# Kernel optimization log

Measured on AMD Instinct MI355X. Metric: run time of the kernel, lower is better.

Reference implementation:

```python
import jax, jax.numpy as jnp
import numpy as np

DIM, HEADS, DEPTH, SEQ, LOCAL_W = 1024, 16, 7, 2048, 64
HEAD_DIM = DIM // HEADS
SCALE = 1.0 / HEAD_DIM ** 0.5


def cantor_mask(S, depth, local_window):
    """Allowed (i,j): |i-j| within local window, OR |i-j| lies in the Cantor set
    under `depth` levels of ternary subdivision (no base-3 digit equals 1)."""
    idx = np.arange(S)
    d = np.abs(idx[:, None] - idx[None, :])
    x = d.copy()
    ok = np.ones_like(d, dtype=bool)
    for _ in range(depth):
        ok &= (x % 3) != 1
        x //= 3
    ok &= x == 0  # offset must be < 3**depth
    return jnp.asarray(ok | (d <= local_window))  # [S, S] bool


def setup_inputs() -> dict:
    key = jax.random.key(0)
    ks = jax.random.split(key, 8)
    B = 2
    s = 0.02
    return {
        "query": jax.random.normal(ks[0], (B, SEQ, DIM), jnp.float32),
        "key_value": jax.random.normal(ks[1], (B, SEQ, DIM), jnp.float32),
        "Wq": jax.random.normal(ks[2], (DIM, DIM), jnp.float32) * s,
        "bq": jnp.zeros((DIM,), jnp.float32),
        "Wkv": jax.random.normal(ks[3], (DIM, 2 * DIM), jnp.float32) * s,
        "bkv": jnp.zeros((2 * DIM,), jnp.float32),
        "Wo": jax.random.normal(ks[4], (DIM, DIM), jnp.float32) * s,
        "bo": jnp.zeros((DIM,), jnp.float32),
    }


def reference(query, key_value, Wq, bq, Wkv, bkv, Wo, bo):
    B, S, D = query.shape
    H, hd = HEADS, HEAD_DIM
    mask = cantor_mask(S, DEPTH, LOCAL_W)  # static [S, S] bool

    q = (query @ Wq + bq).reshape(B, S, H, hd).transpose(0, 2, 1, 3)  # [B,H,S,hd]
    kv = (key_value @ Wkv + bkv).reshape(B, S, 2, H, hd).transpose(2, 0, 3, 1, 4)
    k, v = kv[0], kv[1]  # [B,H,S,hd]

    scores = jnp.einsum("bhqd,bhkd->bhqk", q, k) * SCALE
    scores = jnp.where(mask, scores, jnp.finfo(scores.dtype).min)
    attn = jax.nn.softmax(scores, axis=-1)
    out = jnp.einsum("bhqk,bhkd->bhqd", attn, v)  # [B,H,S,hd]
    out = out.transpose(0, 2, 1, 3).reshape(B, S, D)
    return out @ Wo + bo
```

## Files before the change

kernel.cpp:

```cpp
#include <hip/hip_runtime.h>
#include <stdint.h>

typedef _Float16 half_t;
typedef __attribute__((ext_vector_type(8))) _Float16 half8;
typedef __attribute__((ext_vector_type(4))) _Float16 half4;
typedef __attribute__((ext_vector_type(4))) float floatx4;

#define SEQ 2048
#define NH 16
#define HD 64

#define MFMA16(a, b, c) __builtin_amdgcn_mfma_f32_16x16x16f16(a, b, c, 0, 0, 0)
#define MFMA32K(a, b, c) __builtin_amdgcn_mfma_f32_16x16x32_f16(a, b, c, 0, 0, 0)

#define QSCALE 0.1803368801111306f

__global__ __launch_bounds__(256) void prep(
    const float* __restrict__ query, const float* __restrict__ key_value,
    const float* __restrict__ Wq, const float* __restrict__ Wkv,
    const float* __restrict__ Wo, half_t* __restrict__ xq,
    half_t* __restrict__ xkv, half_t* __restrict__ wqT,
    half_t* __restrict__ wkvT, half_t* __restrict__ woT,
    uint8_t* __restrict__ tok, uint8_t* __restrict__ tok16,
    uint64_t* __restrict__ maskw) {
  int bx = blockIdx.x, tid = threadIdx.x;
  if (bx < 8192) {
    const float* s; half_t* d; int i;
    if (bx < 4096) { s = query; d = xq; i = (bx * 256 + tid) * 4; }
    else { s = key_value; d = xkv; i = ((bx - 4096) * 256 + tid) * 4; }
    floatx4 v = *(const floatx4*)(s + i);
    half4 h;
    h[0] = (half_t)v[0]; h[1] = (half_t)v[1];
    h[2] = (half_t)v[2]; h[3] = (half_t)v[3];
    *(half4*)(d + i) = h;
    return;
  }
  if (bx < 12288) {
    __shared__ float tile[32][33];
    int id = bx - 8192;
    const float* W; half_t* Wt; int N, nt, kt;
    if (id < 1024) { W = Wq; Wt = wqT; N = 1024; nt = id & 31; kt = id >> 5; }
    else if (id < 3072) { int i2 = id - 1024; W = Wkv; Wt = wkvT; N = 2048; nt = i2 & 63; kt = i2 >> 6; }
    else { int i2 = id - 3072; W = Wo; Wt = woT; N = 1024; nt = i2 & 31; kt = i2 >> 5; }
    const int K = 1024;
    int n0 = nt * 32, k0 = kt * 32;
    int tx = tid & 31, ty = tid >> 5;
#pragma unroll
    for (int i = 0; i < 4; ++i)
      tile[ty + i * 8][tx] = W[(size_t)(k0 + ty + i * 8) * N + n0 + tx];
    __syncthreads();
#pragma unroll
    for (int i = 0; i < 4; ++i)
      Wt[(size_t)(n0 + ty + i * 8) * K + k0 + tx] = (half_t)tile[tx][ty + i * 8];
    return;
  }
  __shared__ uint8_t slut[2048];
  int ib = bx - 12288;
  for (int d = tid; d < 2048; d += 256) {
    int x = d;
    bool ok = true;
    for (int it = 0; it < 7; ++it) { ok &= ((x % 3) != 1); x /= 3; }
    ok &= (x == 0);
    slut[d] = (ok || d <= 64) ? 1 : 0;
  }
  __syncthreads();
  if (ib == 0) {
    if (tid < 64) {
      int delta = tid - 32;
      int lo = delta * 64 - 63, hi = delta * 64 + 63;
      uint8_t any = 0;
      for (int x = lo; x <= hi; ++x) {
        int a = x < 0 ? -x : x;
        if (a < 2048) any |= slut[a];
      }
      tok[tid] = any;
    }
    {
      int d16 = tid - 128;
      int ctr = d16 * 16;
      uint8_t any = 0;
      for (int x = ctr - 15; x <= ctr + 15; ++x) {
        int a = x < 0 ? -x : x;
        if (a < 2048) any |= slut[a];
      }
      tok16[tid] = any;
    }
  }
  int g = ib * 256 + tid;
  int tt = g - 2048;
  uint64_t w = 0;
  for (int jj = 0; jj < 64; ++jj) {
    int d = tt - jj; d = d < 0 ? -d : d;
    if (d < 2048 && slut[d]) w |= (1ull << jj);
  }
  maskw[g] = w;
}

__device__ __forceinline__ void cp16(half_t* lds, const half_t* g) {
  __builtin_amdgcn_global_load_lds(
      (const __attribute__((address_space(1))) uint32_t*)g,
      (__attribute__((address_space(3))) uint32_t*)lds, 16, 0, 0);
}

__global__ __launch_bounds__(256) void gemm_qkv(
    const half_t* __restrict__ xq, const half_t* __restrict__ xkv,
    const half_t* __restrict__ wqT, const half_t* __restrict__ wkvT,
    const float* __restrict__ bq, const float* __restrict__ bkv,
    half_t* __restrict__ qout, half_t* __restrict__ kout,
    half_t* __restrict__ vTout) {
  extern __shared__ char smemraw[];
  half_t* As = (half_t*)smemraw;
  half_t* Bs = As + 8192;
  const int K = 1024;
  bool isq = blockIdx.y < 8;
  const half_t* A = isq ? xq : xkv;
  const half_t* Bt = isq ? wqT : wkvT;
  const float* bias = isq ? bq : bkv;
  int n0 = (isq ? blockIdx.y : (blockIdx.y - 8)) * 128;
  int m0 = blockIdx.x * 128;

  int tid = threadIdx.x;
  int wave = tid >> 6, lane = tid & 63;
  int c = lane & 15, quad = lane >> 4;
  int wm = (wave >> 1) * 64, wn = (wave & 1) * 64;

  floatx4 acc[4][4] = {};
  int arow = tid >> 2, akc = (tid & 3) * 8;

  cp16(&As[wave * 512], A + (size_t)(m0 + arow) * K + akc);
  cp16(&As[2048 + wave * 512], A + (size_t)(m0 + 64 + arow) * K + akc);
  cp16(&Bs[wave * 512], Bt + (size_t)(n0 + arow) * K + akc);
  cp16(&Bs[2048 + wave * 512], Bt + (size_t)(n0 + 64 + arow) * K + akc);

  for (int kt = 0; kt < 32; ++kt) {
    __syncthreads();
    if (kt + 1 < 32) {
      int k0 = (kt + 1) * 32;
      int b = (kt + 1) & 1;
      cp16(&As[b * 4096 + wave * 512], A + (size_t)(m0 + arow) * K + k0 + akc);
      cp16(&As[b * 4096 + 2048 + wave * 512], A + (size_t)(m0 + 64 + arow) * K + k0 + akc);
      cp16(&Bs[b * 4096 + wave * 512], Bt + (size_t)(n0 + arow) * K + k0 + akc);
      cp16(&Bs[b * 4096 + 2048 + wave * 512], Bt + (size_t)(n0 + 64 + arow) * K + k0 + akc);
    }
    int b = kt & 1;
    half8 af[4], bf[4];
#pragma unroll
    for (int mt = 0; mt < 4; ++mt)
      af[mt] = *(const half8*)&As[b * 4096 + (wm + mt * 16 + c) * 32 + quad * 8];
#pragma unroll
    for (int nt = 0; nt < 4; ++nt)
      bf[nt] = *(const half8*)&Bs[b * 4096 + (wn + nt * 16 + c) * 32 + quad * 8];
#pragma unroll
    for (int mt = 0; mt < 4; ++mt)
#pragma unroll
      for (int nt = 0; nt < 4; ++nt)
        acc[mt][nt] = MFMA32K(af[mt], bf[nt], acc[mt][nt]);
  }

  __syncthreads();
  half_t* ep = (half_t*)smemraw;
  int bb = m0 >> 11, sbase = m0 & 2047;
  bool isv = (!isq) && (n0 >= 1024);

  if (!isv) {
#pragma unroll
    for (int nt = 0; nt < 4; ++nt) {
      int nl = wn + nt * 16 + c;
      float bv = bias[n0 + nl];
#pragma unroll
      for (int mt = 0; mt < 4; ++mt)
#pragma unroll
        for (int r = 0; r < 4; ++r) {
          int ml = wm + mt * 16 + quad * 4 + r;
          float v = acc[mt][nt][r] + bv;
          if (isq) v *= QSCALE;
          ep[ml * 128 + nl] = (half_t)v;
        }
    }
    __syncthreads();
    half_t* outp = isq ? qout : kout;
#pragma unroll
    for (int rd = 0; rd < 8; ++rd) {
      int id = rd * 256 + tid;
      int ml = id >> 4, ch = id & 15;
      int ng = n0 + ch * 8;
      int h = ng >> 6, d0 = ng & 63;
      half8 v = *(const half8*)&ep[ml * 128 + ch * 8];
      *(half8*)(outp + ((size_t)(bb * 16 + h) * SEQ + sbase + ml) * 64 + d0) = v;
    }
  } else {
#pragma unroll
    for (int nt = 0; nt < 4; ++nt) {
      int nl = wn + nt * 16 + c;
      float bv = bias[n0 + nl];
#pragma unroll
      for (int mt = 0; mt < 4; ++mt) {
        int ml = wm + mt * 16 + quad * 4;
        half4 hv;
#pragma unroll
        for (int r = 0; r < 4; ++r) hv[r] = (half_t)(acc[mt][nt][r] + bv);
        *(half4*)&ep[nl * 136 + ml] = hv;
      }
    }
    __syncthreads();
#pragma unroll
    for (int rd = 0; rd < 8; ++rd) {
      int id = rd * 256 + tid;
      int nl = id >> 4, mc = id & 15;
      int ng = n0 + nl;
      int h = (ng >> 6) & 15, d = ng & 63;
      half8 v = *(const half8*)&ep[nl * 136 + mc * 8];
      *(half8*)(vTout + ((size_t)(bb * 16 + h) * 64 + d) * SEQ + sbase + mc * 8) = v;
    }
  }
}

__global__ __launch_bounds__(256) void gemm_out(
    const half_t* __restrict__ A, const half_t* __restrict__ Bt,
    const float* __restrict__ bias, float* __restrict__ outf) {
  __shared__ half_t As[2][128 * 32];
  __shared__ half_t Bs[2][64 * 32];
  const int K = 1024;
  int tid = threadIdx.x;
  int wave = tid >> 6, lane = tid & 63;
  int c = lane & 15, quad = lane >> 4;
  int wm = (wave >> 1) * 64, wn = (wave & 1) * 32;
  int m0 = blockIdx.x * 128, n0 = blockIdx.y * 64;

  floatx4 acc[4][2] = {};
  int arow = tid >> 2, akc = (tid & 3) * 8;

  cp16(&As[0][wave * 512], A + (size_t)(m0 + arow) * K + akc);
  cp16(&As[0][2048 + wave * 512], A + (size_t)(m0 + 64 + arow) * K + akc);
  cp16(&Bs[0][wave * 512], Bt + (size_t)(n0 + arow) * K + akc);

  for (int kt = 0; kt < 32; ++kt) {
    __syncthreads();
    if (kt + 1 < 32) {
      int k0 = (kt + 1) * 32;
      int b = (kt + 1) & 1;
      cp16(&As[b][wave * 512], A + (size_t)(m0 + arow) * K + k0 + akc);
      cp16(&As[b][2048 + wave * 512], A + (size_t)(m0 + 64 + arow) * K + k0 + akc);
      cp16(&Bs[b][wave * 512], Bt + (size_t)(n0 + arow) * K + k0 + akc);
    }
    int b = kt & 1;
    half8 af[4], bf[2];
#pragma unroll
    for (int mt = 0; mt < 4; ++mt)
      af[mt] = *(const half8*)&As[b][(wm + mt * 16 + c) * 32 + quad * 8];
#pragma unroll
    for (int nt = 0; nt < 2; ++nt)
      bf[nt] = *(const half8*)&Bs[b][(wn + nt * 16 + c) * 32 + quad * 8];
#pragma unroll
    for (int mt = 0; mt < 4; ++mt)
#pragma unroll
      for (int nt = 0; nt < 2; ++nt)
        acc[mt][nt] = MFMA32K(af[mt], bf[nt], acc[mt][nt]);
  }

#pragma unroll
  for (int nt = 0; nt < 2; ++nt) {
    int n = n0 + wn + nt * 16 + c;
    float bv = bias[n];
#pragma unroll
    for (int mt = 0; mt < 4; ++mt)
#pragma unroll
      for (int r = 0; r < 4; ++r) {
        int m = m0 + wm + mt * 16 + quad * 4 + r;
        outf[(size_t)m * 1024 + n] = acc[mt][nt][r] + bv;
      }
  }
}

__global__ __launch_bounds__(256) void attn_kernel(
    const half_t* __restrict__ qb, const half_t* __restrict__ kb,
    const half_t* __restrict__ vTg, half_t* __restrict__ ctx,
    const uint64_t* __restrict__ maskw, const uint8_t* __restrict__ tok,
    const uint8_t* __restrict__ tok16g) {
  __shared__ half_t kT[64 * 64];
  __shared__ half_t vT[64 * 64];
  __shared__ half_t ot[64 * 72];
  __shared__ int list[34];
  __shared__ uint8_t tok16s[256];

  int tid = threadIdx.x, wave = tid >> 6, lane = tid & 63;
  int c = lane & 15, q = lane >> 4;
  int i0 = blockIdx.x * 64;
  int bh = blockIdx.y;
  const half_t* qbase = qb + (size_t)bh * SEQ * HD;
  const half_t* kg = kb + (size_t)bh * SEQ * HD;
  const half_t* vg = vTg + (size_t)bh * HD * SEQ;

  tok16s[tid] = tok16g[tid];
  if (wave == 0) {
    int jt = lane;
    bool act = (jt < 32) && tok[(jt - (i0 >> 6)) + 32];
    unsigned long long bal = __ballot(act);
    if (act) {
      int pre = __popcll(bal & ((1ull << jt) - 1));
      list[1 + pre] = jt << 6;
    }
    if (lane == 0) list[0] = __popcll(bal);
  }

  int i_row = i0 + wave * 16 + c;
  int it16 = (i0 >> 4) + wave;
  half8 qf0 = *(const half8*)(qbase + (size_t)i_row * 64 + q * 8);
  half8 qf1 = *(const half8*)(qbase + (size_t)i_row * 64 + 32 + q * 8);

  floatx4 oacc[4] = {};
  floatx4 lacc = {};
  half4 ones;
  ones[0] = (half_t)1.f; ones[1] = (half_t)1.f;
  ones[2] = (half_t)1.f; ones[3] = (half_t)1.f;

  int srow = tid >> 2;
  int sch = (tid & 3) * 2;
  int ssw = srow & 7;

  __syncthreads();
  int nact = list[0];
  int j0 = list[1];

  half8 kr0 = *(const half8*)(kg + (size_t)(j0 + srow) * 64 + sch * 8);
  half8 kr1 = *(const half8*)(kg + (size_t)(j0 + srow) * 64 + sch * 8 + 8);
  half8 vr0 = *(const half8*)(vg + (size_t)srow * SEQ + j0 + sch * 8);
  half8 vr1 = *(const half8*)(vg + (size_t)srow * SEQ + j0 + sch * 8 + 8);

  for (int ti = 0; ti < nact; ++ti) {
    uint64_t w = maskw[(i_row - j0) + 2048];
    int bidx = (j0 >> 4) - it16 + 128;
    __syncthreads();
    *(half8*)&kT[srow * 64 + ((sch ^ ssw) * 8)] = kr0;
    *(half8*)&kT[srow * 64 + (((sch + 1) ^ ssw) * 8)] = kr1;
    *(half8*)&vT[srow * 64 + ((sch ^ ssw) * 8)] = vr0;
    *(half8*)&vT[srow * 64 + (((sch + 1) ^ ssw) * 8)] = vr1;
    int j0n = j0;
    if (ti + 1 < nact) {
      j0n = list[2 + ti];
      kr0 = *(const half8*)(kg + (size_t)(j0n + srow) * 64 + sch * 8);
      kr1 = *(const half8*)(kg + (size_t)(j0n + srow) * 64 + sch * 8 + 8);
      vr0 = *(const half8*)(vg + (size_t)srow * SEQ + j0n + sch * 8);
      vr1 = *(const half8*)(vg + (size_t)srow * SEQ + j0n + sch * 8 + 8);
    }
    __syncthreads();

    uint32_t wlo = (uint32_t)(w >> (4 * q));
    uint32_t whi = (uint32_t)(w >> (32 + 4 * q));
#pragma unroll
    for (int jt = 0; jt < 4; ++jt) {
      if (!tok16s[bidx + jt]) continue;
      int row = jt * 16 + c;
      int sw = c & 7;
      half8 a0 = *(const half8*)&kT[row * 64 + ((q ^ sw) * 8)];
      half8 a1 = *(const half8*)&kT[row * 64 + (((4 + q) ^ sw) * 8)];
      floatx4 t = {};
      t = MFMA32K(a0, qf0, t);
      t = MFMA32K(a1, qf1, t);
      uint32_t ww = (jt < 2) ? wlo : whi;
#pragma unroll
      for (int r = 0; r < 4; ++r) {
        float p = __builtin_exp2f(t[r]);
        int bitpos = 16 * (jt & 1) + r;
        uint32_t msk = (uint32_t)(((int)(ww << (31 - bitpos))) >> 31);
        t[r] = __uint_as_float(__float_as_uint(p) & msk);
      }
      auto lo = __builtin_amdgcn_cvt_pkrtz(t[0], t[1]);
      auto hi = __builtin_amdgcn_cvt_pkrtz(t[2], t[3]);
      half4 pb;
      pb[0] = lo[0]; pb[1] = lo[1]; pb[2] = hi[0]; pb[3] = hi[1];
      lacc = MFMA16(ones, pb, lacc);
#pragma unroll
      for (int mt = 0; mt < 4; ++mt) {
        int drow = mt * 16 + c;
        int ch = 2 * jt + (q >> 1);
        half4 a = *(const half4*)&vT[drow * 64 + ((ch ^ sw) * 8) + (q & 1) * 4];
        oacc[mt] = MFMA16(a, pb, oacc[mt]);
      }
    }
    j0 = j0n;
  }

  float inv_l = 1.0f / lacc[0];
#pragma unroll
  for (int mt = 0; mt < 4; ++mt)
#pragma unroll
    for (int r = 0; r < 4; ++r)
      ot[(wave * 16 + c) * 72 + mt * 16 + 4 * q + r] = (half_t)(oacc[mt][r] * inv_l);
  __syncthreads();
  {
    int row = tid >> 2, chq = tid & 3;
    int b = bh >> 4, h = bh & 15;
    size_t base = (((size_t)(b * SEQ + i0 + row) * NH) + h) * 64 + chq * 16;
    half8 v0 = *(const half8*)&ot[row * 72 + chq * 16];
    half8 v1 = *(const half8*)&ot[row * 72 + chq * 16 + 8];
    *(half8*)(ctx + base) = v0;
    *(half8*)(ctx + base + 8) = v1;
  }
}

extern "C" void kernel_launch(void* const* d_in, const int* in_sizes, int n_in,
                              void* d_out, int out_size, void* d_ws, size_t ws_size,
                              hipStream_t stream) {
  const float* query = (const float*)d_in[0];
  const float* key_value = (const float*)d_in[1];
  const float* Wq = (const float*)d_in[2];
  const float* bq = (const float*)d_in[3];
  const float* Wkv = (const float*)d_in[4];
  const float* bkv = (const float*)d_in[5];
  const float* Wo = (const float*)d_in[6];
  const float* bo = (const float*)d_in[7];

  char* ws = (char*)d_ws;
  uint8_t* tok = (uint8_t*)ws;
  uint8_t* tok16 = (uint8_t*)(ws + 1024);
  uint64_t* maskw = (uint64_t*)(ws + 4096);
  const size_t MB = 1ull << 20;
  half_t* xq = (half_t*)(ws + 1 * MB);
  half_t* xkv = (half_t*)(ws + 9 * MB);
  half_t* wqT = (half_t*)(ws + 17 * MB);
  half_t* wkvT = (half_t*)(ws + 19 * MB);
  half_t* woT = (half_t*)(ws + 23 * MB);
  half_t* qbuf = (half_t*)(ws + 25 * MB);
  half_t* kbuf = (half_t*)(ws + 33 * MB);
  half_t* vTg = (half_t*)(ws + 41 * MB);
  half_t* ctx = xq;

  hipLaunchKernelGGL(prep, dim3(12304), dim3(256), 0, stream,
                     query, key_value, Wq, Wkv, Wo, xq, xkv, wqT, wkvT, woT,
                     tok, tok16, maskw);
  hipLaunchKernelGGL(gemm_qkv, dim3(32, 24), dim3(256), 34816, stream,
                     xq, xkv, wqT, wkvT, bq, bkv, qbuf, kbuf, vTg);
  hipLaunchKernelGGL(attn_kernel, dim3(32, 32), dim3(256), 0, stream,
                     qbuf, kbuf, vTg, ctx, maskw, tok, tok16);
  hipLaunchKernelGGL(gemm_out, dim3(32, 16), dim3(256), 0, stream,
                     ctx, woT, bo, (float*)d_out);
}
```

Before: 226.3 us.

## Widen attention tiles to 128 queries and coarsen prep kernel blocks

The attention kernel now runs 512 threads (8 waves) per block covering 128 query rows, so each K/V tile loaded into shared memory is reused by twice as many query rows. The active-tile list becomes the union of the two 64-row query groups' tile sets. The grid is flattened with a head-interleaved block ordering. The prep kernel also processes several elements or transpose tiles per block, which cuts the block count. In exchange, some waves may iterate over K tiles that are fully masked for their rows, and occupancy per CU may change.

New measurement: 211.5 us. -6.5%, faster.

```diff
diff --git a/kernel.cpp b/kernel.cpp
--- a/kernel.cpp
+++ b/kernel.cpp
@@ -24,38 +24,46 @@
     uint8_t* __restrict__ tok, uint8_t* __restrict__ tok16,
     uint64_t* __restrict__ maskw) {
   int bx = blockIdx.x, tid = threadIdx.x;
-  if (bx < 8192) {
-    const float* s; half_t* d; int i;
-    if (bx < 4096) { s = query; d = xq; i = (bx * 256 + tid) * 4; }
-    else { s = key_value; d = xkv; i = ((bx - 4096) * 256 + tid) * 4; }
-    floatx4 v = *(const floatx4*)(s + i);
-    half4 h;
-    h[0] = (half_t)v[0]; h[1] = (half_t)v[1];
-    h[2] = (half_t)v[2]; h[3] = (half_t)v[3];
-    *(half4*)(d + i) = h;
+  if (bx < 2048) {
+    const float* s; half_t* d; int base;
+    if (bx < 1024) { s = query; d = xq; base = bx * 4096; }
+    else { s = key_value; d = xkv; base = (bx - 1024) * 4096; }
+#pragma unroll
+    for (int u = 0; u < 4; ++u) {
+      int i = base + u * 1024 + tid * 4;
+      floatx4 v = *(const floatx4*)(s + i);
+      half4 h;
+      h[0] = (half_t)v[0]; h[1] = (half_t)v[1];
+      h[2] = (half_t)v[2]; h[3] = (half_t)v[3];
+      *(half4*)(d + i) = h;
+    }
     return;
   }
-  if (bx < 12288) {
+  if (bx < 4096) {
     __shared__ float tile[32][33];
-    int id = bx - 8192;
-    const float* W; half_t* Wt; int N, nt, kt;
-    if (id < 1024) { W = Wq; Wt = wqT; N = 1024; nt = id & 31; kt = id >> 5; }
-    else if (id < 3072) { int i2 = id - 1024; W = Wkv; Wt = wkvT; N = 2048; nt = i2 & 63; kt = i2 >> 6; }
-    else { int i2 = id - 3072; W = Wo; Wt = woT; N = 1024; nt = i2 & 31; kt = i2 >> 5; }
+    int tx = tid & 31, ty = tid >> 5;
     const int K = 1024;
-    int n0 = nt * 32, k0 = kt * 32;
-    int tx = tid & 31, ty = tid >> 5;
-#pragma unroll
-    for (int i = 0; i < 4; ++i)
-      tile[ty + i * 8][tx] = W[(size_t)(k0 + ty + i * 8) * N + n0 + tx];
-    __syncthreads();
-#pragma unroll
-    for (int i = 0; i < 4; ++i)
-      Wt[(size_t)(n0 + ty + i * 8) * K + k0 + tx] = (half_t)tile[tx][ty + i * 8];
+#pragma unroll
+    for (int u = 0; u < 2; ++u) {
+      int t = (bx - 2048) * 2 + u;
+      const float* W; half_t* Wt; int N, nt, kt;
+      if (t < 1024) { W = Wq; Wt = wqT; N = 1024; nt = t & 31; kt = t >> 5; }
+      else if (t < 3072) { int t2 = t - 1024; W = Wkv; Wt = wkvT; N = 2048; nt = t2 & 63; kt = t2 >> 6; }
+      else { int t2 = t - 3072; W = Wo; Wt = woT; N = 1024; nt = t2 & 31; kt = t2 >> 5; }
+      int n0 = nt * 32, k0 = kt * 32;
+#pragma unroll
+      for (int i = 0; i < 4; ++i)
+        tile[ty + i * 8][tx] = W[(size_t)(k0 + ty + i * 8) * N + n0 + tx];
+      __syncthreads();
+#pragma unroll
+      for (int i = 0; i < 4; ++i)
+        Wt[(size_t)(n0 + ty + i * 8) * K + k0 + tx] = (half_t)tile[tx][ty + i * 8];
+      __syncthreads();
+    }
     return;
   }
   __shared__ uint8_t slut[2048];
-  int ib = bx - 12288;
+  int ib = bx - 4096;
   for (int d = tid; d < 2048; d += 256) {
     int x = d;
     bool ok = true;
@@ -272,29 +280,33 @@
   }
 }
 
-__global__ __launch_bounds__(256) void attn_kernel(
+__global__ __launch_bounds__(512) void attn_kernel(
     const half_t* __restrict__ qb, const half_t* __restrict__ kb,
     const half_t* __restrict__ vTg, half_t* __restrict__ ctx,
     const uint64_t* __restrict__ maskw, const uint8_t* __restrict__ tok,
     const uint8_t* __restrict__ tok16g) {
   __shared__ half_t kT[64 * 64];
   __shared__ half_t vT[64 * 64];
-  __shared__ half_t ot[64 * 72];
+  __shared__ half_t ot[128 * 72];
   __shared__ int list[34];
   __shared__ uint8_t tok16s[256];
 
   int tid = threadIdx.x, wave = tid >> 6, lane = tid & 63;
   int c = lane & 15, q = lane >> 4;
-  int i0 = blockIdx.x * 64;
-  int bh = blockIdx.y;
+  int id = blockIdx.x;
+  int bh = (id & 7) * 4 + ((id >> 3) & 3);
+  int it128 = id >> 5;
+  int i0 = it128 << 7;
   const half_t* qbase = qb + (size_t)bh * SEQ * HD;
   const half_t* kg = kb + (size_t)bh * SEQ * HD;
   const half_t* vg = vTg + (size_t)bh * HD * SEQ;
 
-  tok16s[tid] = tok16g[tid];
+  if (tid < 256) tok16s[tid] = tok16g[tid];
   if (wave == 0) {
     int jt = lane;
-    bool act = (jt < 32) && tok[(jt - (i0 >> 6)) + 32];
+    int base = i0 >> 6;
+    bool act = (jt < 32) &&
+               (tok[(jt - base) + 32] | tok[(jt - base - 1) + 32]);
     unsigned long long bal = __ballot(act);
     if (act) {
       int pre = __popcll(bal & ((1ull << jt) - 1));
@@ -314,34 +326,28 @@
   ones[0] = (half_t)1.f; ones[1] = (half_t)1.f;
   ones[2] = (half_t)1.f; ones[3] = (half_t)1.f;
 
-  int srow = tid >> 2;
-  int sch = (tid & 3) * 2;
+  int srow = tid >> 3;
+  int sch = tid & 7;
   int ssw = srow & 7;
 
   __syncthreads();
   int nact = list[0];
   int j0 = list[1];
 
-  half8 kr0 = *(const half8*)(kg + (size_t)(j0 + srow) * 64 + sch * 8);
-  half8 kr1 = *(const half8*)(kg + (size_t)(j0 + srow) * 64 + sch * 8 + 8);
-  half8 vr0 = *(const half8*)(vg + (size_t)srow * SEQ + j0 + sch * 8);
-  half8 vr1 = *(const half8*)(vg + (size_t)srow * SEQ + j0 + sch * 8 + 8);
+  half8 kr = *(const half8*)(kg + (size_t)(j0 + srow) * 64 + sch * 8);
+  half8 vr = *(const half8*)(vg + (size_t)srow * SEQ + j0 + sch * 8);
 
   for (int ti = 0; ti < nact; ++ti) {
     uint64_t w = maskw[(i_row - j0) + 2048];
     int bidx = (j0 >> 4) - it16 + 128;
     __syncthreads();
-    *(half8*)&kT[srow * 64 + ((sch ^ ssw) * 8)] = kr0;
-    *(half8*)&kT[srow * 64 + (((sch + 1) ^ ssw) * 8)] = kr1;
-    *(half8*)&vT[srow * 64 + ((sch ^ ssw) * 8)] = vr0;
-    *(half8*)&vT[srow * 64 + (((sch + 1) ^ ssw) * 8)] = vr1;
+    *(half8*)&kT[srow * 64 + ((sch ^ ssw) * 8)] = kr;
+    *(half8*)&vT[srow * 64 + ((sch ^ ssw) * 8)] = vr;
     int j0n = j0;
     if (ti + 1 < nact) {
       j0n = list[2 + ti];
-      kr0 = *(const half8*)(kg + (size_t)(j0n + srow) * 64 + sch * 8);
-      kr1 = *(const half8*)(kg + (size_t)(j0n + srow) * 64 + sch * 8 + 8);
-      vr0 = *(const half8*)(vg + (size_t)srow * SEQ + j0n + sch * 8);
-      vr1 = *(const half8*)(vg + (size_t)srow * SEQ + j0n + sch * 8 + 8);
+      kr = *(const half8*)(kg + (size_t)(j0n + srow) * 64 + sch * 8);
+      vr = *(const half8*)(vg + (size_t)srow * SEQ + j0n + sch * 8);
     }
     __syncthreads();
 
@@ -426,12 +432,12 @@
   half_t* vTg = (half_t*)(ws + 41 * MB);
   half_t* ctx = xq;
 
-  hipLaunchKernelGGL(prep, dim3(12304), dim3(256), 0, stream,
+  hipLaunchKernelGGL(prep, dim3(4112), dim3(256), 0, stream,
                      query, key_value, Wq, Wkv, Wo, xq, xkv, wqT, wkvT, woT,
                      tok, tok16, maskw);
   hipLaunchKernelGGL(gemm_qkv, dim3(32, 24), dim3(256), 34816, stream,
                      xq, xkv, wqT, wkvT, bq, bkv, qbuf, kbuf, vTg);
-  hipLaunchKernelGGL(attn_kernel, dim3(32, 32), dim3(256), 0, stream,
+  hipLaunchKernelGGL(attn_kernel, dim3(512), dim3(512), 0, stream,
                      qbuf, kbuf, vTg, ctx, maskw, tok, tok16);
   hipLaunchKernelGGL(gemm_out, dim3(32, 16), dim3(256), 0, stream,
                      ctx, woT, bo, (float*)d_out);
```
